# Kernel tuning notes

Hardware: AMD Instinct MI355X
Metric: run time of the kernel (lower is better)

## Reference

```python
import jax, jax.numpy as jnp
import numpy as np

D_MODEL = 256

def setup_inputs() -> dict:
    key = jax.random.key(0)
    k1, k2, k3, k4, k5, k6 = jax.random.split(key, 6)
    B, LQ, LK, D = 16, 2048, 2048, D_MODEL
    q = jax.random.normal(k1, (B, LQ, D), dtype=jnp.float32)
    k = jax.random.normal(k2, (B, LK, D), dtype=jnp.float32)
    tsp = jax.random.normal(k3, (B, LK, D), dtype=jnp.float32)
    # xavier_uniform for w_qk [D, D] (no bias)
    bound = float(np.sqrt(6.0 / (D + D)))
    w_qk = jax.random.uniform(k4, (D, D), minval=-bound, maxval=bound, dtype=jnp.float32)
    # linear1: default torch init kaiming-uniform-ish; any values fine for correctness baseline
    lim = float(1.0 / np.sqrt(D))
    w1 = jax.random.uniform(k5, (D, D), minval=-lim, maxval=lim, dtype=jnp.float32)
    b1 = jax.random.uniform(k6, (D,), minval=-lim, maxval=lim, dtype=jnp.float32)
    return {"q": q, "k": k, "tsp": tsp, "w_qk": w_qk, "w1": w1, "b1": b1}

def reference(q, k, tsp, w_qk, w1, b1):
    d_head = q.shape[-1]
    temperature = jnp.asarray(np.power(d_head, 0.5), dtype=q.dtype)
    residual = q
    # shared Q/K projection (torch Linear: x @ W^T)
    qp = jnp.einsum('bqd,ed->bqe', q, w_qk)            # [B, Lq, Dh]
    kp = jnp.einsum('bkd,ed->bke', k, w_qk)            # [B, Lk, Dh]
    logits = jnp.einsum('bqd,bkd->bqk', qp, kp) / temperature  # [B, Lq, Lk]
    attn = jax.nn.softmax(logits, axis=2)
    # sigmoid is monotonic: max(sigmoid(x)) == sigmoid(max(x))
    prob_fg = jax.nn.sigmoid(jnp.max(logits, axis=-1, keepdims=True))  # [B, Lq, 1]
    out = jnp.einsum('bqk,bkd->bqd', attn, tsp)        # [B, Lq, Dh]
    gated = (residual + out) * prob_fg
    return jnp.einsum('bqd,ed->bqe', gated, w1) + b1
```

## Files before the change

kernel.cpp:

```cpp
#include <hip/hip_runtime.h>
#include <hip/hip_bf16.h>

typedef __bf16 bf16;
typedef __bf16 bf16x8 __attribute__((ext_vector_type(8)));
typedef __bf16 bf16x4 __attribute__((ext_vector_type(4)));
typedef __bf16 bf16x2 __attribute__((ext_vector_type(2)));
typedef float f32x4 __attribute__((ext_vector_type(4)));

static __device__ __forceinline__ f32x4 mfma16(bf16x8 a, bf16x8 b, f32x4 c) {
    return __builtin_amdgcn_mfma_f32_16x16x32_bf16(a, b, c, 0, 0, 0);
}

static __device__ __forceinline__ void load16_to_lds(const void* g, void* l) {
    __builtin_amdgcn_global_load_lds(
        (const __attribute__((address_space(1))) unsigned int*)g,
        (__attribute__((address_space(3))) unsigned int*)l, 16, 0, 0);
}

#define LKV 2048
#define DM 256

template<bool IN_BF16, bool OUT_BF16, bool HAS_BIAS>
static __device__ __forceinline__ void gemm_body(char* smem,
                                                 const void* __restrict__ Xv,
                                                 const float* __restrict__ Wf,
                                                 const float* __restrict__ bias,
                                                 float scale, void* __restrict__ Y,
                                                 long rowbase) {
    bf16* Xl  = (bf16*)smem;
    char* WlB = smem + 33792;
    const int tid  = threadIdx.x;
    const int lane = tid & 63, wave = tid >> 6;
    const int hi = lane >> 4, lo = lane & 15;

    if (IN_BF16) {
        const bf16* Xb = (const bf16*)Xv;
#pragma unroll
        for (int i = 0; i < 8; ++i) {
            int idx = i * 256 + tid;
            int r = idx >> 5, c8 = (idx & 31) * 8;
            uint4 v = *(const uint4*)(Xb + (rowbase + r) * 256 + c8);
            *(uint4*)(Xl + r * 264 + c8) = v;
        }
    } else {
        const float* X = (const float*)Xv;
#pragma unroll
        for (int i = 0; i < 16; ++i) {
            int idx4 = i * 256 + tid;
            int e = idx4 * 4;
            int r = e >> 8, c = e & 255;
            float4 v = *(const float4*)(X + (rowbase + r) * 256 + c);
            bf16x4 o;
            o[0] = (bf16)v.x; o[1] = (bf16)v.y; o[2] = (bf16)v.z; o[3] = (bf16)v.w;
            *(bf16x4*)(Xl + r * 264 + c) = o;
        }
    }

    f32x4 acc[16];
    const f32x4 zero = {0.f, 0.f, 0.f, 0.f};
#pragma unroll
    for (int n = 0; n < 16; ++n) acc[n] = zero;

    for (int ks = 0; ks < 8; ++ks) {
        __syncthreads();
#pragma unroll
        for (int c = 0; c < 8; ++c) {
            int idx = c * 256 + tid;
            int e = idx >> 3, q4 = (idx & 7) * 4;
            float4 v = *(const float4*)(Wf + e * 256 + ks * 32 + q4);
            bf16x4 o;
            o[0] = (bf16)v.x; o[1] = (bf16)v.y; o[2] = (bf16)v.z; o[3] = (bf16)v.w;
            *(bf16x4*)(WlB + e * 80 + q4 * 2) = o;
        }
        __syncthreads();
        bf16x8 a = *(const bf16x8*)((const char*)Xl + (wave * 16 + lo) * 528 + ks * 64 + hi * 16);
#pragma unroll
        for (int n = 0; n < 16; ++n) {
            bf16x8 bfr = *(const bf16x8*)(WlB + (n * 16 + lo) * 80 + hi * 16);
            acc[n] = mfma16(a, bfr, acc[n]);
        }
    }

#pragma unroll
    for (int n = 0; n < 16; ++n) {
        int col = n * 16 + lo;
        float bv = HAS_BIAS ? bias[col] : 0.f;
#pragma unroll
        for (int r = 0; r < 4; ++r) {
            long row = rowbase + wave * 16 + hi * 4 + r;
            float v = acc[n][r] * scale + bv;
            if (OUT_BF16) ((bf16*)Y)[row * 256 + col] = (bf16)v;
            else          ((float*)Y)[row * 256 + col] = v;
        }
    }
}

__global__ __launch_bounds__(256) void prep_qk(const float* __restrict__ q,
                                               const float* __restrict__ k,
                                               const float* __restrict__ wqk,
                                               const float* __restrict__ tsp,
                                               bf16* __restrict__ qp,
                                               bf16* __restrict__ kp,
                                               bf16* __restrict__ tspF) {
    __shared__ __align__(16) char smem[54272];
    const int tid = threadIdx.x;
    int bid = (int)blockIdx.x;
    if (bid < 1024) {
        bool is_k = bid >= 512;
        gemm_body<false, true, false>(smem, is_k ? k : q, wqk, nullptr,
                                      is_k ? 1.0f : 0.0625f, is_k ? kp : qp,
                                      (long)(bid & 511) * 64);
        return;
    }
    int id = bid - 1024;
    const int b = id >> 7;
    const int kv0 = (id & 31) * 64, d0 = ((id >> 5) & 3) * 64;
    float (*tile)[65] = (float(*)[65])smem;
#pragma unroll
    for (int i = 0; i < 4; ++i) {
        int idx = i * 256 + tid;
        int kv = idx >> 4, c4 = (idx & 15) * 4;
        float4 v = *(const float4*)(tsp + ((long)(b * LKV + kv0 + kv)) * DM + d0 + c4);
        tile[kv][c4 + 0] = v.x; tile[kv][c4 + 1] = v.y;
        tile[kv][c4 + 2] = v.z; tile[kv][c4 + 3] = v.w;
    }
    __syncthreads();
    char* outb = (char*)tspF + ((long)b << 20);
#pragma unroll
    for (int i = 0; i < 2; ++i) {
        int w = i * 256 + tid;
        int ti = w >> 8;
        int dti = (w >> 6) & 3;
        int lane = w & 63;
        int hi = lane >> 4, lo = lane & 15;
        bf16x8 o;
#pragma unroll
        for (int j = 0; j < 8; ++j) o[j] = (bf16)tile[ti * 32 + hi * 8 + j][dti * 16 + lo];
        int t_abs = (kv0 >> 5) + ti;
        int dt_abs = (d0 >> 4) + dti;
        *(bf16x8*)(outb + (((t_abs * 16 + dt_abs) << 6) + lane) * 16) = o;
    }
}

__global__ __launch_bounds__(256) void gemm_out(const bf16* __restrict__ gated,
                                                const float* __restrict__ w1,
                                                const float* __restrict__ b1,
                                                float* __restrict__ out) {
    __shared__ __align__(16) char smem[54272];
    gemm_body<true, false, true>(smem, gated, w1, b1, 1.0f, out, (long)blockIdx.x * 64);
}

__global__ __launch_bounds__(256, 2) void flash6(const bf16* __restrict__ qp,
                                                 const bf16* __restrict__ kp,
                                                 const bf16* __restrict__ tspF,
                                                 const float* __restrict__ qorig,
                                                 bf16* __restrict__ gated) {
    __shared__ __align__(16) char kbuf[3][16384];
    const int tid  = threadIdx.x;
    const int lane = tid & 63, wave = tid >> 6;
    const int hi = lane >> 4, lo = lane & 15;

    int id  = (int)blockIdx.x;
    int bid = (id & 7) * 64 + (id >> 3);
    const int b  = bid >> 5;
    const int qb = bid & 31;
    const long qbase = (long)b * LKV + qb * 64;
    const char* kp_g  = (const char*)(kp + (long)b * LKV * DM);
    const char* tsp_f = (const char*)tspF + ((long)b << 20) + lane * 16;

    int kp_off[4];
#pragma unroll
    for (int j = 0; j < 4; ++j) {
        int kv = wave * 8 + j * 2 + (lane >> 5);
        kp_off[j] = kv * 512 + (((lane & 31) ^ (kv & 7)) << 4);
    }

    int bp_src[4];
#pragma unroll
    for (int k2 = 0; k2 < 4; ++k2)
        bp_src[k2] = ((((hi & 1) * 2 + (k2 >> 1)) << 4) + lo) << 2;

    bf16x8 aq[8];
    {
        const bf16* qrow = qp + (qbase + wave * 16 + lo) * DM;
#pragma unroll
        for (int ks = 0; ks < 8; ++ks) aq[ks] = *(const bf16x8*)(qrow + ks * 32 + hi * 8);
    }

    bf16x8 ones;
#pragma unroll
    for (int j = 0; j < 8; ++j) ones[j] = (bf16)1.0f;

    f32x4 o[16], o_l;
    const f32x4 zero = {0.f, 0.f, 0.f, 0.f};
#pragma unroll
    for (int n = 0; n < 16; ++n) o[n] = zero;
    o_l = zero;
    float m = -1e30f, tm = -1e30f;

    const int kswz = (lo & 7) << 4;

#pragma unroll
    for (int j = 0; j < 4; ++j)
        load16_to_lds(kp_g + kp_off[j],          &kbuf[0][wave * 4096 + j * 1024]);
#pragma unroll
    for (int j = 0; j < 4; ++j)
        load16_to_lds(kp_g + 16384 + kp_off[j],  &kbuf[1][wave * 4096 + j * 1024]);

    for (int t = 0; t < 64; ++t) {
        if (t == 0)       { asm volatile("s_waitcnt vmcnt(4)"  ::: "memory"); }
        else if (t == 63) { asm volatile("s_waitcnt vmcnt(16)" ::: "memory"); }
        else              { asm volatile("s_waitcnt vmcnt(20)" ::: "memory"); }
        __builtin_amdgcn_sched_barrier(0);
        __builtin_amdgcn_s_barrier();
        __builtin_amdgcn_sched_barrier(0);

        bf16x8 tt[16];
        {
            const char* tb = tsp_f + (long)t * 16384;
#pragma unroll
            for (int dt = 0; dt < 16; ++dt)
                tt[dt] = *(const bf16x8*)(tb + dt * 1024);
        }
        if (t < 62) {
            const int dslot = (t + 2) % 3;
            const char* src = kp_g + (long)(t + 2) * 16384;
#pragma unroll
            for (int j = 0; j < 4; ++j)
                load16_to_lds(src + kp_off[j], &kbuf[dslot][wave * 4096 + j * 1024]);
        }
        __builtin_amdgcn_sched_barrier(0);

        f32x4 s[2];
        const char* kb = kbuf[t % 3];
        __builtin_amdgcn_s_setprio(1);
#pragma unroll
        for (int n = 0; n < 2; ++n) {
            s[n] = zero;
            const char* rowp = kb + ((n * 16 + lo) << 9);
#pragma unroll
            for (int ks = 0; ks < 8; ++ks) {
                bf16x8 kk = *(const bf16x8*)(rowp + ((ks * 64 + hi * 16) ^ kswz));
                s[n] = mfma16(kk, aq[ks], s[n]);
            }
        }
        __builtin_amdgcn_s_setprio(0);

        float pm = fmaxf(fmaxf(fmaxf(s[0][0], s[0][1]), fmaxf(s[0][2], s[0][3])),
                         fmaxf(fmaxf(s[1][0], s[1][1]), fmaxf(s[1][2], s[1][3])));
        pm = fmaxf(pm, __shfl_xor(pm, 16));
        pm = fmaxf(pm, __shfl_xor(pm, 32));
        tm = fmaxf(tm, pm);
        if (__any(pm > m + 8.f)) {
            float nm = fmaxf(m, pm);
            float a = __expf(m - nm);
            m = nm;
            o_l *= a;
#pragma unroll
            for (int n = 0; n < 16; ++n) o[n] *= a;
        }
        int cvt[2][2];
#pragma unroll
        for (int n = 0; n < 2; ++n)
#pragma unroll
            for (int c = 0; c < 2; ++c) {
                bf16x2 pr;
                pr[0] = (bf16)__expf(s[n][2 * c]     - m);
                pr[1] = (bf16)__expf(s[n][2 * c + 1] - m);
                cvt[n][c] = __builtin_bit_cast(int, pr);
            }
        int pki[4];
#pragma unroll
        for (int k2 = 0; k2 < 4; ++k2) {
            int a0 = __builtin_amdgcn_ds_bpermute(bp_src[k2], cvt[0][k2 & 1]);
            int a1 = __builtin_amdgcn_ds_bpermute(bp_src[k2], cvt[1][k2 & 1]);
            pki[k2] = (hi < 2) ? a0 : a1;
        }
        int4 pii = make_int4(pki[0], pki[1], pki[2], pki[3]);
        bf16x8 pk = __builtin_bit_cast(bf16x8, pii);

        o_l = mfma16(ones, pk, o_l);
        __builtin_amdgcn_s_setprio(1);
#pragma unroll
        for (int dt = 0; dt < 16; ++dt)
            o[dt] = mfma16(tt[dt], pk, o[dt]);
        __builtin_amdgcn_s_setprio(0);
    }

    float prob = 1.f / (1.f + __expf(-tm));
    float invl = 1.f / o_l[0];
    long row = qbase + wave * 16 + lo;
#pragma unroll
    for (int dt = 0; dt < 16; ++dt) {
        int c0 = dt * 16 + hi * 4;
        float4 qv = *(const float4*)(qorig + row * 256 + c0);
        bf16x4 g;
        g[0] = (bf16)((qv.x + o[dt][0] * invl) * prob);
        g[1] = (bf16)((qv.y + o[dt][1] * invl) * prob);
        g[2] = (bf16)((qv.z + o[dt][2] * invl) * prob);
        g[3] = (bf16)((qv.w + o[dt][3] * invl) * prob);
        *(bf16x4*)(gated + row * 256 + c0) = g;
    }
}

extern "C" void kernel_launch(void* const* d_in, const int* in_sizes, int n_in,
                              void* d_out, int out_size, void* d_ws, size_t ws_size,
                              hipStream_t stream) {
    const float* q    = (const float*)d_in[0];
    const float* k    = (const float*)d_in[1];
    const float* tsp  = (const float*)d_in[2];
    const float* w_qk = (const float*)d_in[3];
    const float* w1   = (const float*)d_in[4];
    const float* b1   = (const float*)d_in[5];
    float* out = (float*)d_out;
    char* ws = (char*)d_ws;

    bf16* qp_b  = (bf16*)(ws + 0);
    bf16* kp_b  = (bf16*)(ws + 16777216);
    bf16* tspF  = (bf16*)(ws + 33554432);
    bf16* gated = (bf16*)(ws + 50331648);

    prep_qk<<<3072, 256, 0, stream>>>(q, k, w_qk, tsp, qp_b, kp_b, tspF);

    flash6<<<512, 256, 0, stream>>>(qp_b, kp_b, tspF, q, gated);

    gemm_out<<<512, 256, 0, stream>>>(gated, w1, b1, out);
}
```

Baseline: 182.4 us.

## Software-pipeline PV MFMA one tile behind QK and switch softmax to exp2

Moves the P·V MFMAs for tile t-1 into the same high-priority block as the QK MFMAs for tile t, so the tensor unit stays busy while the softmax of the current tile is computed. A drain step after the loop finishes the last tile. The tsp and K loads are now issued after the MFMAs, overlapping with the softmax. Also folds log2(e) into the Q scale so exp2f replaces __expf, replaces the ones-vector MFMA row sum with a scalar float sum plus shuffles, and raises the rescale threshold to match the base-2 scale. Costs extra live registers (tt and pk carried across iterations), which risks register pressure at two blocks per CU.

```diff
diff --git a/kernel.cpp b/kernel.cpp
--- a/kernel.cpp
+++ b/kernel.cpp
@@ -108,7 +108,7 @@
     if (bid < 1024) {
         bool is_k = bid >= 512;
         gemm_body<false, true, false>(smem, is_k ? k : q, wqk, nullptr,
-                                      is_k ? 1.0f : 0.0625f, is_k ? kp : qp,
+                                      is_k ? 1.0f : 0.09016844f, is_k ? kp : qp,
                                       (long)(bid & 511) * 64);
         return;
     }
@@ -131,14 +131,14 @@
         int w = i * 256 + tid;
         int ti = w >> 8;
         int dti = (w >> 6) & 3;
-        int lane = w & 63;
-        int hi = lane >> 4, lo = lane & 15;
+        int fl = w & 63;
+        int hi = fl >> 4, lo = fl & 15;
         bf16x8 o;
 #pragma unroll
         for (int j = 0; j < 8; ++j) o[j] = (bf16)tile[ti * 32 + hi * 8 + j][dti * 16 + lo];
         int t_abs = (kv0 >> 5) + ti;
         int dt_abs = (d0 >> 4) + dti;
-        *(bf16x8*)(outb + (((t_abs * 16 + dt_abs) << 6) + lane) * 16) = o;
+        *(bf16x8*)(outb + (((t_abs * 16 + dt_abs) << 6) + fl) * 16) = o;
     }
 }
 
@@ -150,11 +150,11 @@
     gemm_body<true, false, true>(smem, gated, w1, b1, 1.0f, out, (long)blockIdx.x * 64);
 }
 
-__global__ __launch_bounds__(256, 2) void flash6(const bf16* __restrict__ qp,
-                                                 const bf16* __restrict__ kp,
-                                                 const bf16* __restrict__ tspF,
-                                                 const float* __restrict__ qorig,
-                                                 bf16* __restrict__ gated) {
+__global__ __launch_bounds__(256, 2) void flash12(const bf16* __restrict__ qp,
+                                                  const bf16* __restrict__ kp,
+                                                  const bf16* __restrict__ tspF,
+                                                  const float* __restrict__ qorig,
+                                                  bf16* __restrict__ gated) {
     __shared__ __align__(16) char kbuf[3][16384];
     const int tid  = threadIdx.x;
     const int lane = tid & 63, wave = tid >> 6;
@@ -174,11 +174,11 @@
         int kv = wave * 8 + j * 2 + (lane >> 5);
         kp_off[j] = kv * 512 + (((lane & 31) ^ (kv & 7)) << 4);
     }
-
     int bp_src[4];
 #pragma unroll
     for (int k2 = 0; k2 < 4; ++k2)
         bp_src[k2] = ((((hi & 1) * 2 + (k2 >> 1)) << 4) + lo) << 2;
+    const int kswz = (lo & 7) << 4;
 
     bf16x8 aq[8];
     {
@@ -187,18 +187,15 @@
         for (int ks = 0; ks < 8; ++ks) aq[ks] = *(const bf16x8*)(qrow + ks * 32 + hi * 8);
     }
 
-    bf16x8 ones;
-#pragma unroll
-    for (int j = 0; j < 8; ++j) ones[j] = (bf16)1.0f;
-
-    f32x4 o[16], o_l;
+    f32x4 o[16];
     const f32x4 zero = {0.f, 0.f, 0.f, 0.f};
 #pragma unroll
     for (int n = 0; n < 16; ++n) o[n] = zero;
-    o_l = zero;
-    float m = -1e30f, tm = -1e30f;
-
-    const int kswz = (lo & 7) << 4;
+    float m = -1e30f, tm = -1e30f, l = 0.f;
+    bf16x8 pk;
+#pragma unroll
+    for (int j = 0; j < 8; ++j) pk[j] = (bf16)0.0f;
+    bf16x8 tt[16];
 
 #pragma unroll
     for (int j = 0; j < 4; ++j)
@@ -215,60 +212,63 @@
         __builtin_amdgcn_s_barrier();
         __builtin_amdgcn_sched_barrier(0);
 
-        bf16x8 tt[16];
-        {
-            const char* tb = tsp_f + (long)t * 16384;
-#pragma unroll
-            for (int dt = 0; dt < 16; ++dt)
-                tt[dt] = *(const bf16x8*)(tb + dt * 1024);
-        }
-        if (t < 62) {
-            const int dslot = (t + 2) % 3;
-            const char* src = kp_g + (long)(t + 2) * 16384;
-#pragma unroll
-            for (int j = 0; j < 4; ++j)
-                load16_to_lds(src + kp_off[j], &kbuf[dslot][wave * 4096 + j * 1024]);
-        }
-        __builtin_amdgcn_sched_barrier(0);
-
-        f32x4 s[2];
+        f32x4 s0 = zero, s1 = zero;
         const char* kb = kbuf[t % 3];
         __builtin_amdgcn_s_setprio(1);
 #pragma unroll
-        for (int n = 0; n < 2; ++n) {
-            s[n] = zero;
-            const char* rowp = kb + ((n * 16 + lo) << 9);
-#pragma unroll
-            for (int ks = 0; ks < 8; ++ks) {
-                bf16x8 kk = *(const bf16x8*)(rowp + ((ks * 64 + hi * 16) ^ kswz));
-                s[n] = mfma16(kk, aq[ks], s[n]);
-            }
+        for (int ks = 0; ks < 8; ++ks) {
+            bf16x8 k0 = *(const bf16x8*)(kb + (lo << 9) + ((ks * 64 + hi * 16) ^ kswz));
+            bf16x8 k1 = *(const bf16x8*)(kb + ((16 + lo) << 9) + ((ks * 64 + hi * 16) ^ kswz));
+            s0 = mfma16(k0, aq[ks], s0);
+            s1 = mfma16(k1, aq[ks], s1);
+        }
+        if (t > 0) {
+#pragma unroll
+            for (int dt = 0; dt < 16; ++dt)
+                o[dt] = mfma16(tt[dt], pk, o[dt]);
         }
         __builtin_amdgcn_s_setprio(0);
 
-        float pm = fmaxf(fmaxf(fmaxf(s[0][0], s[0][1]), fmaxf(s[0][2], s[0][3])),
-                         fmaxf(fmaxf(s[1][0], s[1][1]), fmaxf(s[1][2], s[1][3])));
+        {
+            const char* ttb = tsp_f + (long)t * 16384;
+#pragma unroll
+            for (int dt = 0; dt < 16; ++dt)
+                tt[dt] = *(const bf16x8*)(ttb + dt * 1024);
+        }
+        if (t < 62) {
+            const char* src = kp_g + (long)(t + 2) * 16384;
+            char* dst = &kbuf[(t + 2) % 3][wave * 4096];
+#pragma unroll
+            for (int j = 0; j < 4; ++j)
+                load16_to_lds(src + kp_off[j], dst + j * 1024);
+        }
+
+        float pm = fmaxf(fmaxf(fmaxf(s0[0], s0[1]), fmaxf(s0[2], s0[3])),
+                         fmaxf(fmaxf(s1[0], s1[1]), fmaxf(s1[2], s1[3])));
         pm = fmaxf(pm, __shfl_xor(pm, 16));
         pm = fmaxf(pm, __shfl_xor(pm, 32));
         tm = fmaxf(tm, pm);
-        if (__any(pm > m + 8.f)) {
+        if (__any(pm > m + 11.5f)) {
             float nm = fmaxf(m, pm);
-            float a = __expf(m - nm);
+            float a = exp2f(m - nm);
             m = nm;
-            o_l *= a;
+            l *= a;
 #pragma unroll
             for (int n = 0; n < 16; ++n) o[n] *= a;
         }
+        float p0 = exp2f(s0[0] - m), p1 = exp2f(s0[1] - m);
+        float p2 = exp2f(s0[2] - m), p3 = exp2f(s0[3] - m);
+        float p4 = exp2f(s1[0] - m), p5 = exp2f(s1[1] - m);
+        float p6 = exp2f(s1[2] - m), p7 = exp2f(s1[3] - m);
+        l += (p0 + p1) + (p2 + p3) + (p4 + p5) + (p6 + p7);
         int cvt[2][2];
-#pragma unroll
-        for (int n = 0; n < 2; ++n)
-#pragma unroll
-            for (int c = 0; c < 2; ++c) {
-                bf16x2 pr;
-                pr[0] = (bf16)__expf(s[n][2 * c]     - m);
-                pr[1] = (bf16)__expf(s[n][2 * c + 1] - m);
-                cvt[n][c] = __builtin_bit_cast(int, pr);
-            }
+        {
+            bf16x2 pr;
+            pr[0] = (bf16)p0; pr[1] = (bf16)p1; cvt[0][0] = __builtin_bit_cast(int, pr);
+            pr[0] = (bf16)p2; pr[1] = (bf16)p3; cvt[0][1] = __builtin_bit_cast(int, pr);
+            pr[0] = (bf16)p4; pr[1] = (bf16)p5; cvt[1][0] = __builtin_bit_cast(int, pr);
+            pr[0] = (bf16)p6; pr[1] = (bf16)p7; cvt[1][1] = __builtin_bit_cast(int, pr);
+        }
         int pki[4];
 #pragma unroll
         for (int k2 = 0; k2 < 4; ++k2) {
@@ -277,18 +277,17 @@
             pki[k2] = (hi < 2) ? a0 : a1;
         }
         int4 pii = make_int4(pki[0], pki[1], pki[2], pki[3]);
-        bf16x8 pk = __builtin_bit_cast(bf16x8, pii);
-
-        o_l = mfma16(ones, pk, o_l);
-        __builtin_amdgcn_s_setprio(1);
-#pragma unroll
-        for (int dt = 0; dt < 16; ++dt)
-            o[dt] = mfma16(tt[dt], pk, o[dt]);
-        __builtin_amdgcn_s_setprio(0);
-    }
-
-    float prob = 1.f / (1.f + __expf(-tm));
-    float invl = 1.f / o_l[0];
+        pk = __builtin_bit_cast(bf16x8, pii);
+    }
+
+#pragma unroll
+    for (int dt = 0; dt < 16; ++dt)
+        o[dt] = mfma16(tt[dt], pk, o[dt]);
+
+    l += __shfl_xor(l, 16);
+    l += __shfl_xor(l, 32);
+    float prob = 1.f / (1.f + __expf(-tm * 0.69314718f));
+    float invl = 1.f / l;
     long row = qbase + wave * 16 + lo;
 #pragma unroll
     for (int dt = 0; dt < 16; ++dt) {
@@ -322,7 +321,7 @@
 
     prep_qk<<<3072, 256, 0, stream>>>(q, k, w_qk, tsp, qp_b, kp_b, tspF);
 
-    flash6<<<512, 256, 0, stream>>>(qp_b, kp_b, tspF, q, gated);
+    flash12<<<512, 256, 0, stream>>>(qp_b, kp_b, tspF, q, gated);
 
     gemm_out<<<512, 256, 0, stream>>>(gated, w1, b1, out);
 }
```

After: 167.4 us. 1.09x faster.
